# Kernel optimization log

Measured on AMD Instinct MI355X. Metric: run time of the kernel, lower is better.

Reference implementation:

```python
import jax, jax.numpy as jnp
import numpy as np
import math

B, S, H, NH = 2, 2048, 1024, 16
HD = H // NH


def setup_inputs() -> dict:
    key = jax.random.key(0)
    k1, k2, k3 = jax.random.split(key, 3)
    hidden_states = jax.random.normal(k1, (B, S, H), dtype=jnp.float32)
    attention_mask = jnp.zeros((B, 1, 1, S), dtype=jnp.float32)
    w_qkv = jax.random.normal(k2, (3 * H, H), dtype=jnp.float32) * (1.0 / math.sqrt(H))
    w_out = jax.random.normal(k3, (H, H), dtype=jnp.float32) * (1.0 / math.sqrt(H))
    gate = jnp.ones((NH,), dtype=jnp.float32)
    return {"hidden_states": hidden_states, "attention_mask": attention_mask,
            "w_qkv": w_qkv, "w_out": w_out, "gate": gate}


def reference(hidden_states, attention_mask, w_qkv, w_out, gate):
    b, s, h = hidden_states.shape
    nh, hd = NH, HD
    # fused QKV projection (no bias)
    qkv = hidden_states @ w_qkv.T                      # [b, s, 3h]
    qkv = qkv.reshape(b, s, 3, nh, hd)
    q, k, v = jnp.moveaxis(qkv, 2, 0)                  # each [b, s, nh, hd]
    q = q.transpose(0, 2, 1, 3)                        # [b, nh, s, hd]
    k = k.transpose(0, 2, 1, 3)
    v = v.transpose(0, 2, 1, 3)
    scores = jnp.einsum('bhqd,bhkd->bhqk', q, k) / math.sqrt(hd)
    scores = scores + attention_mask                   # broadcast [b,1,1,s]
    probs = jax.nn.softmax(scores, axis=-1)            # dropout p=0 -> identity
    ctx = jnp.einsum('bhqk,bhkd->bhqd', probs, v)      # [b, nh, s, hd]
    ctx = ctx.transpose(0, 2, 1, 3)                    # [b, s, nh, hd]
    ctx = ctx * gate[None, None, :, None]              # per-head gating
    ctx = ctx.reshape(b, s, h)
    out = ctx @ w_out.T
    # all gates active (> 1e-4) -> active_gates/num_heads == 1, no rescale
    return out
```

## Files before the change

### kernel.cpp

```cpp
#include <hip/hip_runtime.h>
#include <stdint.h>


typedef __attribute__((ext_vector_type(8))) short short8;
typedef __attribute__((ext_vector_type(4))) float floatx4;
typedef __attribute__((ext_vector_type(4))) unsigned int uint4v;
typedef __attribute__((ext_vector_type(2))) unsigned int uint2v;

__device__ __forceinline__ unsigned short f2bf(float f) {
    unsigned int u = __float_as_uint(f);
    unsigned int r = u + 0x7fffu + ((u >> 16) & 1u);
    return (unsigned short)(r >> 16);
}
#if __has_builtin(__builtin_amdgcn_cvt_pk_bf16_f32)
__device__ __forceinline__ unsigned int pack_bf2(float lo, float hi) {
    auto v = __builtin_amdgcn_cvt_pk_bf16_f32(lo, hi);
    return __builtin_bit_cast(unsigned int, v);
}
#else
__device__ __forceinline__ unsigned int pack_bf2(float lo, float hi) {
    unsigned int a = __float_as_uint(lo) + 0x8000u;
    unsigned int b = __float_as_uint(hi) + 0x8000u;
    return __builtin_amdgcn_perm(b, a, 0x07060302u);
}
#endif

#if __has_builtin(__builtin_amdgcn_exp2f)
#define EXP2(x) __builtin_amdgcn_exp2f(x)
#else
#define EXP2(x) exp2f(x)
#endif

__device__ __forceinline__ void gl2lds16(const void* g, void* l) {
    __builtin_amdgcn_global_load_lds(
        (const __attribute__((address_space(1))) unsigned int*)g,
        (__attribute__((address_space(3))) unsigned int*)l, 16, 0, 0);
}

#define MFMA32(a, b, c) __builtin_amdgcn_mfma_f32_16x16x32_bf16((a), (b), (c), 0, 0, 0)

__global__ __launch_bounds__(256)
void cvt_all(const float* __restrict__ a, const float* __restrict__ b,
             const float* __restrict__ c, const float* __restrict__ mask,
             unsigned short* __restrict__ oa, unsigned short* __restrict__ ob,
             unsigned short* __restrict__ oc, float* __restrict__ m2b)
{
    int i = blockIdx.x * 256 + threadIdx.x;
    if (i >= 2097152) {
        int off = i - 2097152;
        float4 v = *(const float4*)(mask + (size_t)off * 4);
        const float L2E = 1.44269504f, C2 = -14.4269504f;
        float4 w;
        w.x = fmaf(v.x, L2E, C2); w.y = fmaf(v.y, L2E, C2);
        w.z = fmaf(v.z, L2E, C2); w.w = fmaf(v.w, L2E, C2);
        *(float4*)(m2b + (size_t)off * 4) = w;
        return;
    }
    const float* src; unsigned short* dst; int off;
    if (i < 1048576)      { src = a; dst = oa; off = i; }
    else if (i < 1835008) { src = b; dst = ob; off = i - 1048576; }
    else                  { src = c; dst = oc; off = i - 1835008; }
    float4 v = *(const float4*)(src + (size_t)off * 4);
    uint2v w;
    w[0] = pack_bf2(v.x, v.y);
    w[1] = pack_bf2(v.z, v.w);
    *(uint2v*)(dst + (size_t)off * 4) = w;
}

template<int MODE, int BN, int WAVES>
__global__ __launch_bounds__(WAVES * 64)
void gemm_nt(const unsigned short* __restrict__ A,
             const unsigned short* __restrict__ Bm,
             unsigned short* __restrict__ out0,
             unsigned short* __restrict__ out1,
             unsigned short* __restrict__ out2,
             float* __restrict__ outf,
             int N)
{
    constexpr int BUFB  = 8192 + BN * 64;
    constexpr int NSTEP = 32;
    constexpr int NA    = 8 / WAVES;
    constexpr int NB    = BN / (16 * WAVES);
    constexpr int BSL   = BN / 32;
    constexpr int MI    = 16 / WAVES;
    __shared__ unsigned char smem[3 * BUFB];
    const int K = 1024;
    const int tid  = threadIdx.x;
    const int wave = tid >> 6, lane = tid & 63;
    const int l15  = lane & 15, quad = lane >> 4;
    const int wm = wave >> 1, wn = wave & 1;

    int Lid = blockIdx.y * gridDim.x + blockIdx.x;
    int bm = (Lid & 7) * 4 + ((Lid >> 3) & 3);
    int bn = Lid >> 5;

    floatx4 acc[MI][BSL];
#pragma unroll
    for (int i = 0; i < MI; i++)
#pragma unroll
        for (int j = 0; j < BSL; j++)
            acc[i][j] = floatx4{0.f, 0.f, 0.f, 0.f};

    int soffA[NA], soffB[NB];
#pragma unroll
    for (int l = 0; l < NA; l++) {
        int s = (wave * NA + l) * 64 + lane;
        int L = s >> 3, q = (s & 7) ^ (L & 7);
        soffA[l] = (L * 2 + (q >> 2)) * K + (q & 3) * 8;
    }
#pragma unroll
    for (int l = 0; l < NB; l++) {
        int s = (wave * NB + l) * 64 + lane;
        int L = s >> 3, q = (s & 7) ^ (L & 7);
        soffB[l] = (L * 2 + (q >> 2)) * K + (q & 3) * 8;
    }
    int aoff[MI], boff[BSL];
#pragma unroll
    for (int i = 0; i < MI; i++) {
        int r = wm * (MI * 16) + i * 16 + l15, L = r >> 1;
        aoff[i] = L * 128 + (((((r & 1) << 2) | quad) ^ (L & 7)) * 16);
    }
#pragma unroll
    for (int j = 0; j < BSL; j++) {
        int r = wn * (BN / 2) + j * 16 + l15, L = r >> 1;
        boff[j] = 8192 + L * 128 + (((((r & 1) << 2) | quad) ^ (L & 7)) * 16);
    }

    const unsigned short* Abase = A  + (size_t)(bm * 128) * K;
    const unsigned short* Bbase = Bm + (size_t)(bn * BN) * K;

    auto STAGE = [&](int u, int bufb) {
        const int k0 = u * 32;
#pragma unroll
        for (int l = 0; l < NA; l++)
            gl2lds16(Abase + (size_t)soffA[l] + k0, &smem[bufb + (wave * NA + l) * 1024]);
#pragma unroll
        for (int l = 0; l < NB; l++)
            gl2lds16(Bbase + (size_t)soffB[l] + k0, &smem[bufb + 8192 + (wave * NB + l) * 1024]);
    };

    STAGE(0, 0);
    STAGE(1, BUFB);

    int b0 = 0, b2 = 2;
    for (int t = 0; t < NSTEP; t++) {
        asm volatile("" ::: "memory");
        __builtin_amdgcn_s_barrier();
        asm volatile("" ::: "memory");
        if (t + 2 < NSTEP) {
            STAGE(t + 2, b2 * BUFB);
            if (NA + NB == 2) asm volatile("s_waitcnt vmcnt(4)" ::: "memory");
            else              asm volatile("s_waitcnt vmcnt(6)" ::: "memory");
        } else if (t + 2 == NSTEP) {
            if (NA + NB == 2) asm volatile("s_waitcnt vmcnt(2)" ::: "memory");
            else              asm volatile("s_waitcnt vmcnt(3)" ::: "memory");
        } else {
            asm volatile("s_waitcnt vmcnt(0)" ::: "memory");
        }
        __builtin_amdgcn_s_barrier();
        asm volatile("" ::: "memory");

        const int cb = b0 * BUFB;
        short8 af[MI], bfr[BSL];
#pragma unroll
        for (int i = 0; i < MI; i++)
            af[i] = *(const short8*)(&smem[cb + aoff[i]]);
#pragma unroll
        for (int j = 0; j < BSL; j++)
            bfr[j] = *(const short8*)(&smem[cb + boff[j]]);
#pragma unroll
        for (int i = 0; i < MI; i++)
#pragma unroll
            for (int j = 0; j < BSL; j++)
                acc[i][j] = MFMA32(af[i], bfr[j], acc[i][j]);

        b0 = (b0 == 2) ? 0 : b0 + 1;
        b2 = (b2 == 2) ? 0 : b2 + 1;
    }

#pragma unroll
    for (int i = 0; i < MI; i++) {
#pragma unroll
        for (int j = 0; j < BSL; j++) {
            int n = bn * BN + wn * (BN / 2) + j * 16 + l15;
#pragma unroll
            for (int r = 0; r < 4; r++) {
                int m = bm * 128 + wm * (MI * 16) + i * 16 + quad * 4 + r;
                float fv = acc[i][j][r];
                if (MODE == 1) {
                    outf[(size_t)m * N + n] = fv;
                } else {
                    int t = n >> 10;
                    int h = (n >> 6) & 15;
                    int d = n & 63;
                    int b = m >> 11, si = m & 2047;
                    if (t == 2) {
                        int sip = (si & ~31) | (((si >> 2) & 3) << 3)
                                | (((si >> 4) & 1) << 2) | (si & 3);
                        out2[(((size_t)(b * 16 + h)) * 64 + d) * 2048 + sip] = f2bf(fv);
                    } else {
                        if (t == 0) fv *= 0.18033688f;
                        size_t off = (((size_t)(b * 16 + h)) * 2048 + si) * 64 + d;
                        unsigned short* dst = (t == 0) ? out0 : out1;
                        dst[off] = f2bf(fv);
                    }
                }
            }
        }
    }
}

__global__ __launch_bounds__(256, 2)
void attn_kernel(const unsigned short* __restrict__ Qb,
                 const unsigned short* __restrict__ Kb,
                 const unsigned short* __restrict__ VbT,
                 const float* __restrict__ m2b,
                 const float* __restrict__ gateb,
                 unsigned short* __restrict__ ctx)
{
    __shared__ unsigned char smem[32768];
    const int S = 2048;
    const int tid  = threadIdx.x;
    const int wave = tid >> 6, lane = tid & 63;
    const int l15  = lane & 15, quad = lane >> 4;

    int Lid = blockIdx.y * gridDim.x + blockIdx.x;
    int bh = (Lid & 7) * 4 + ((Lid >> 3) & 3);
    int qc = Lid >> 5;
    const int b = bh >> 4, h = bh & 15;
    const int q0 = qc * 128 + wave * 32;

    const size_t headoff = (size_t)bh * S * 64;
    const unsigned short* Qh  = Qb  + headoff;
    const unsigned short* Kh  = Kb  + headoff;
    const unsigned short* VhT = VbT + headoff;
    const float* m2p = m2b + (size_t)b * S;

    int koff[2], voff[2];
#pragma unroll
    for (int l = 0; l < 2; l++) {
        int s = (wave * 2 + l) * 64 + lane;
        int L = s >> 3, c = (s & 7) ^ (L & 7);
        koff[l] = L * 64 + c * 8;
        voff[l] = L * 2048 + c * 8;
    }
    int qkoff[2];
#pragma unroll
    for (int j = 0; j < 2; j++)
        qkoff[j] = l15 * 128 + (((j * 4 + quad) ^ (l15 & 7)) * 16);

    short8 aq[2][2];
#pragma unroll
    for (int sub = 0; sub < 2; sub++)
#pragma unroll
        for (int s2 = 0; s2 < 2; s2++)
            aq[sub][s2] = *(const short8*)(Qh + (size_t)(q0 + sub * 16 + l15) * 64 + s2 * 32 + quad * 8);

    floatx4 o[2][4];
    floatx4 lq[2];
#pragma unroll
    for (int sub = 0; sub < 2; sub++) {
        lq[sub] = floatx4{0.f, 0.f, 0.f, 0.f};
#pragma unroll
        for (int dt = 0; dt < 4; dt++) o[sub][dt] = floatx4{0.f, 0.f, 0.f, 0.f};
    }

    const uint4v onesu = {0x3F803F80u, 0x3F803F80u, 0x3F803F80u, 0x3F803F80u};
    const short8 ONES = __builtin_bit_cast(short8, onesu);

#pragma unroll
    for (int l = 0; l < 2; l++) {
        gl2lds16(Kh + koff[l], &smem[(wave * 2 + l) * 1024]);
        gl2lds16(VhT + voff[l], &smem[8192 + (wave * 2 + l) * 1024]);
    }

    for (int i = 0; i < 32; i++) {
        const int cb = (i & 1) * 16384;
        const int nb = ((i + 1) & 1) * 16384;
        const int kb = i * 64;
        floatx4 mf[4];
#pragma unroll
        for (int t = 0; t < 4; t++)
            mf[t] = *(const floatx4*)(m2p + kb + t * 16 + quad * 4);
        asm volatile("" ::: "memory");
        __builtin_amdgcn_s_barrier();
        asm volatile("" ::: "memory");
        if (i + 1 < 32) {
            const int kbn = (i + 1) * 64;
#pragma unroll
            for (int l = 0; l < 2; l++) {
                gl2lds16(Kh + (size_t)kbn * 64 + koff[l], &smem[nb + (wave * 2 + l) * 1024]);
                gl2lds16(VhT + kbn + voff[l], &smem[nb + 8192 + (wave * 2 + l) * 1024]);
            }
            asm volatile("s_waitcnt vmcnt(4)" ::: "memory");
        } else {
            asm volatile("s_waitcnt vmcnt(0)" ::: "memory");
        }
        __builtin_amdgcn_s_barrier();
        asm volatile("" ::: "memory");

        short8 kf[4][2];
#pragma unroll
        for (int kt = 0; kt < 4; kt++)
#pragma unroll
            for (int s2 = 0; s2 < 2; s2++)
                kf[kt][s2] = *(const short8*)(&smem[cb + kt * 2048 + qkoff[s2]]);

        floatx4 st[2][4];
        __builtin_amdgcn_s_setprio(1);
#pragma unroll
        for (int sub = 0; sub < 2; sub++)
#pragma unroll
            for (int kt = 0; kt < 4; kt++) {
                st[sub][kt] = MFMA32(kf[kt][0], aq[sub][0], mf[kt]);
                st[sub][kt] = MFMA32(kf[kt][1], aq[sub][1], st[sub][kt]);
            }
        __builtin_amdgcn_s_setprio(0);

        short8 vf[4][2];
#pragma unroll
        for (int dt = 0; dt < 4; dt++)
#pragma unroll
            for (int g = 0; g < 2; g++)
                vf[dt][g] = *(const short8*)(&smem[cb + 8192 + dt * 2048 + qkoff[g]]);

        short8 pf[2][2];
#pragma unroll
        for (int sub = 0; sub < 2; sub++)
#pragma unroll
            for (int g = 0; g < 2; g++) {
                floatx4 a = st[sub][2 * g], c = st[sub][2 * g + 1];
                uint4v pu = {pack_bf2(EXP2(a[0]), EXP2(a[1])),
                             pack_bf2(EXP2(a[2]), EXP2(a[3])),
                             pack_bf2(EXP2(c[0]), EXP2(c[1])),
                             pack_bf2(EXP2(c[2]), EXP2(c[3]))};
                pf[sub][g] = __builtin_bit_cast(short8, pu);
            }

        __builtin_amdgcn_s_setprio(1);
#pragma unroll
        for (int sub = 0; sub < 2; sub++)
#pragma unroll
            for (int g = 0; g < 2; g++) {
#pragma unroll
                for (int dt = 0; dt < 4; dt++)
                    o[sub][dt] = MFMA32(vf[dt][g], pf[sub][g], o[sub][dt]);
                lq[sub] = MFMA32(ONES, pf[sub][g], lq[sub]);
            }
        __builtin_amdgcn_s_setprio(0);
    }

    float g = gateb[h];
#pragma unroll
    for (int sub = 0; sub < 2; sub++) {
        float iv = g / lq[sub][0];
        size_t base = ((size_t)(b * 2048 + q0 + sub * 16 + l15)) * 1024 + h * 64 + quad * 4;
#pragma unroll
        for (int dt = 0; dt < 4; dt++) {
            uint2v w;
            w[0] = pack_bf2(o[sub][dt][0] * iv, o[sub][dt][1] * iv);
            w[1] = pack_bf2(o[sub][dt][2] * iv, o[sub][dt][3] * iv);
            *(uint2v*)(ctx + base + dt * 16) = w;
        }
    }
}

extern "C" void kernel_launch(void* const* d_in, const int* in_sizes, int n_in,
                              void* d_out, int out_size, void* d_ws, size_t ws_size,
                              hipStream_t stream)
{
    const float* hidden = (const float*)d_in[0];
    const float* mask   = (const float*)d_in[1];
    const float* w_qkv  = (const float*)d_in[2];
    const float* w_out  = (const float*)d_in[3];
    const float* gate   = (const float*)d_in[4];
    float* out = (float*)d_out;

    unsigned short* q_buf = (unsigned short*)d_ws;
    unsigned short* k_buf = q_buf + 4194304;
    unsigned short* v_buf = k_buf + 4194304;
    unsigned short* c_buf = v_buf + 4194304;
    unsigned short* h_bf  = c_buf + 4194304;
    unsigned short* wq_bf = h_bf  + 4194304;
    unsigned short* wo_bf = wq_bf + 3145728;
    float* m2_buf = (float*)(wo_bf + 1048576);

    cvt_all<<<8196, 256, 0, stream>>>(hidden, w_qkv, w_out, mask,
                                      h_bf, wq_bf, wo_bf, m2_buf);

    gemm_nt<0, 128, 8><<<dim3(24, 32), 512, 0, stream>>>(h_bf, wq_bf, q_buf, k_buf, v_buf, nullptr, 3072);
    attn_kernel<<<dim3(16, 32), 256, 0, stream>>>(q_buf, k_buf, v_buf, m2_buf, gate, c_buf);
    gemm_nt<1, 64, 4><<<dim3(16, 32), 256, 0, stream>>>(c_buf, wo_bf, nullptr, nullptr, nullptr, out, 1024);
}
```

Baseline: 177.4 us.

## Split attention work across 8 waves with 16 query rows each

After: 183.3 us. +3.3%, slower.

```diff
diff --git a/kernel.cpp b/kernel.cpp
--- a/kernel.cpp
+++ b/kernel.cpp
@@ -210,7 +210,7 @@
     }
 }
 
-__global__ __launch_bounds__(256, 2)
+__global__ __launch_bounds__(512, 4)
 void attn_kernel(const unsigned short* __restrict__ Qb,
                  const unsigned short* __restrict__ Kb,
                  const unsigned short* __restrict__ VbT,
@@ -228,7 +228,7 @@
     int bh = (Lid & 7) * 4 + ((Lid >> 3) & 3);
     int qc = Lid >> 5;
     const int b = bh >> 4, h = bh & 15;
-    const int q0 = qc * 128 + wave * 32;
+    const int q0 = qc * 128 + wave * 16;
 
     const size_t headoff = (size_t)bh * S * 64;
     const unsigned short* Qh  = Qb  + headoff;
@@ -236,43 +236,33 @@
     const unsigned short* VhT = VbT + headoff;
     const float* m2p = m2b + (size_t)b * S;
 
-    int koff[2], voff[2];
-#pragma unroll
-    for (int l = 0; l < 2; l++) {
-        int s = (wave * 2 + l) * 64 + lane;
+    int koff, voff;
+    {
+        int s = wave * 64 + lane;
         int L = s >> 3, c = (s & 7) ^ (L & 7);
-        koff[l] = L * 64 + c * 8;
-        voff[l] = L * 2048 + c * 8;
+        koff = L * 64 + c * 8;
+        voff = L * 2048 + c * 8;
     }
     int qkoff[2];
 #pragma unroll
     for (int j = 0; j < 2; j++)
         qkoff[j] = l15 * 128 + (((j * 4 + quad) ^ (l15 & 7)) * 16);
 
-    short8 aq[2][2];
-#pragma unroll
-    for (int sub = 0; sub < 2; sub++)
-#pragma unroll
-        for (int s2 = 0; s2 < 2; s2++)
-            aq[sub][s2] = *(const short8*)(Qh + (size_t)(q0 + sub * 16 + l15) * 64 + s2 * 32 + quad * 8);
-
-    floatx4 o[2][4];
-    floatx4 lq[2];
-#pragma unroll
-    for (int sub = 0; sub < 2; sub++) {
-        lq[sub] = floatx4{0.f, 0.f, 0.f, 0.f};
-#pragma unroll
-        for (int dt = 0; dt < 4; dt++) o[sub][dt] = floatx4{0.f, 0.f, 0.f, 0.f};
-    }
+    short8 aq[2];
+#pragma unroll
+    for (int s2 = 0; s2 < 2; s2++)
+        aq[s2] = *(const short8*)(Qh + (size_t)(q0 + l15) * 64 + s2 * 32 + quad * 8);
+
+    floatx4 o[4];
+    floatx4 lq = floatx4{0.f, 0.f, 0.f, 0.f};
+#pragma unroll
+    for (int dt = 0; dt < 4; dt++) o[dt] = floatx4{0.f, 0.f, 0.f, 0.f};
 
     const uint4v onesu = {0x3F803F80u, 0x3F803F80u, 0x3F803F80u, 0x3F803F80u};
     const short8 ONES = __builtin_bit_cast(short8, onesu);
 
-#pragma unroll
-    for (int l = 0; l < 2; l++) {
-        gl2lds16(Kh + koff[l], &smem[(wave * 2 + l) * 1024]);
-        gl2lds16(VhT + voff[l], &smem[8192 + (wave * 2 + l) * 1024]);
-    }
+    gl2lds16(Kh + koff, &smem[wave * 1024]);
+    gl2lds16(VhT + voff, &smem[8192 + wave * 1024]);
 
     for (int i = 0; i < 32; i++) {
         const int cb = (i & 1) * 16384;
@@ -287,12 +277,9 @@
         asm volatile("" ::: "memory");
         if (i + 1 < 32) {
             const int kbn = (i + 1) * 64;
-#pragma unroll
-            for (int l = 0; l < 2; l++) {
-                gl2lds16(Kh + (size_t)kbn * 64 + koff[l], &smem[nb + (wave * 2 + l) * 1024]);
-                gl2lds16(VhT + kbn + voff[l], &smem[nb + 8192 + (wave * 2 + l) * 1024]);
-            }
-            asm volatile("s_waitcnt vmcnt(4)" ::: "memory");
+            gl2lds16(Kh + (size_t)kbn * 64 + koff, &smem[nb + wave * 1024]);
+            gl2lds16(VhT + kbn + voff, &smem[nb + 8192 + wave * 1024]);
+            asm volatile("s_waitcnt vmcnt(2)" ::: "memory");
         } else {
             asm volatile("s_waitcnt vmcnt(0)" ::: "memory");
         }
@@ -306,15 +293,13 @@
             for (int s2 = 0; s2 < 2; s2++)
                 kf[kt][s2] = *(const short8*)(&smem[cb + kt * 2048 + qkoff[s2]]);
 
-        floatx4 st[2][4];
+        floatx4 st[4];
         __builtin_amdgcn_s_setprio(1);
 #pragma unroll
-        for (int sub = 0; sub < 2; sub++)
-#pragma unroll
-            for (int kt = 0; kt < 4; kt++) {
-                st[sub][kt] = MFMA32(kf[kt][0], aq[sub][0], mf[kt]);
-                st[sub][kt] = MFMA32(kf[kt][1], aq[sub][1], st[sub][kt]);
-            }
+        for (int kt = 0; kt < 4; kt++) {
+            st[kt] = MFMA32(kf[kt][0], aq[0], mf[kt]);
+            st[kt] = MFMA32(kf[kt][1], aq[1], st[kt]);
+        }
         __builtin_amdgcn_s_setprio(0);
 
         short8 vf[4][2];
@@ -324,44 +309,36 @@
             for (int g = 0; g < 2; g++)
                 vf[dt][g] = *(const short8*)(&smem[cb + 8192 + dt * 2048 + qkoff[g]]);
 
-        short8 pf[2][2];
-#pragma unroll
-        for (int sub = 0; sub < 2; sub++)
-#pragma unroll
-            for (int g = 0; g < 2; g++) {
-                floatx4 a = st[sub][2 * g], c = st[sub][2 * g + 1];
-                uint4v pu = {pack_bf2(EXP2(a[0]), EXP2(a[1])),
-                             pack_bf2(EXP2(a[2]), EXP2(a[3])),
-                             pack_bf2(EXP2(c[0]), EXP2(c[1])),
-                             pack_bf2(EXP2(c[2]), EXP2(c[3]))};
-                pf[sub][g] = __builtin_bit_cast(short8, pu);
-            }
+        short8 pf[2];
+#pragma unroll
+        for (int g = 0; g < 2; g++) {
+            floatx4 a = st[2 * g], c = st[2 * g + 1];
+            uint4v pu = {pack_bf2(EXP2(a[0]), EXP2(a[1])),
+                         pack_bf2(EXP2(a[2]), EXP2(a[3])),
+                         pack_bf2(EXP2(c[0]), EXP2(c[1])),
+                         pack_bf2(EXP2(c[2]), EXP2(c[3]))};
+            pf[g] = __builtin_bit_cast(short8, pu);
+        }
 
         __builtin_amdgcn_s_setprio(1);
 #pragma unroll
-        for (int sub = 0; sub < 2; sub++)
-#pragma unroll
-            for (int g = 0; g < 2; g++) {
-#pragma unroll
-                for (int dt = 0; dt < 4; dt++)
-                    o[sub][dt] = MFMA32(vf[dt][g], pf[sub][g], o[sub][dt]);
-                lq[sub] = MFMA32(ONES, pf[sub][g], lq[sub]);
-            }
+        for (int g = 0; g < 2; g++) {
+#pragma unroll
+            for (int dt = 0; dt < 4; dt++)
+                o[dt] = MFMA32(vf[dt][g], pf[g], o[dt]);
+            lq = MFMA32(ONES, pf[g], lq);
+        }
         __builtin_amdgcn_s_setprio(0);
     }
 
-    float g = gateb[h];
-#pragma unroll
-    for (int sub = 0; sub < 2; sub++) {
-        float iv = g / lq[sub][0];
-        size_t base = ((size_t)(b * 2048 + q0 + sub * 16 + l15)) * 1024 + h * 64 + quad * 4;
-#pragma unroll
-        for (int dt = 0; dt < 4; dt++) {
-            uint2v w;
-            w[0] = pack_bf2(o[sub][dt][0] * iv, o[sub][dt][1] * iv);
-            w[1] = pack_bf2(o[sub][dt][2] * iv, o[sub][dt][3] * iv);
-            *(uint2v*)(ctx + base + dt * 16) = w;
-        }
+    float iv = gateb[h] / lq[0];
+    size_t base = ((size_t)(b * 2048 + q0 + l15)) * 1024 + h * 64 + quad * 4;
+#pragma unroll
+    for (int dt = 0; dt < 4; dt++) {
+        uint2v w;
+        w[0] = pack_bf2(o[dt][0] * iv, o[dt][1] * iv);
+        w[1] = pack_bf2(o[dt][2] * iv, o[dt][3] * iv);
+        *(uint2v*)(ctx + base + dt * 16) = w;
     }
 }
 
@@ -389,6 +366,6 @@
                                       h_bf, wq_bf, wo_bf, m2_buf);
 
     gemm_nt<0, 128, 8><<<dim3(24, 32), 512, 0, stream>>>(h_bf, wq_bf, q_buf, k_buf, v_buf, nullptr, 3072);
-    attn_kernel<<<dim3(16, 32), 256, 0, stream>>>(q_buf, k_buf, v_buf, m2_buf, gate, c_buf);
+    attn_kernel<<<dim3(16, 32), 512, 0, stream>>>(q_buf, k_buf, v_buf, m2_buf, gate, c_buf);
     gemm_nt<1, 64, 4><<<dim3(16, 32), 256, 0, stream>>>(c_buf, wo_bf, nullptr, nullptr, nullptr, out, 1024);
 }
```
